# Kernel tuning notes

Measured on AMD Instinct MI355X. Metric: run time of the kernel, lower is better.

Reference implementation:

```python
import jax, jax.numpy as jnp
import numpy as np

N = 100000          # nodes
E = 1600000         # edges (avg degree 16)
F_NODE = 128        # num_node_features
F_EDGE = 32         # num_edge_features
HID = 128           # hidden_channels
OUT = 64            # out_channels


def setup_inputs() -> dict:
    key = jax.random.key(0)
    k = jax.random.split(key, 8)
    x = jax.random.normal(k[0], (N, F_NODE), dtype=jnp.float32)
    edge_index = jax.random.randint(k[1], (2, E), 0, N, dtype=jnp.int64)
    edge_attr = jax.random.normal(k[2], (E, F_EDGE), dtype=jnp.float32)
    # GCNConv parameters (lin weight + bias), glorot-ish scale
    w1 = jax.random.normal(k[3], (F_NODE + F_EDGE, HID), dtype=jnp.float32) * 0.05
    b1 = jnp.zeros((HID,), dtype=jnp.float32)
    w2 = jax.random.normal(k[4], (HID + F_EDGE, OUT), dtype=jnp.float32) * 0.05
    b2 = jnp.zeros((OUT,), dtype=jnp.float32)
    return {"x": x, "edge_index": edge_index, "edge_attr": edge_attr,
            "w1": w1, "b1": b1, "w2": w2, "b2": b2}


def _gcn_conv(h, src, dst, norm, w, b, num_nodes):
    # PyG GCNConv: linear transform, then normalized gather->scatter aggregation
    h = h @ w                                    # [N, out]
    msg = h[src] * norm[:, None]                 # gather at source nodes [E+N, out]
    out = jax.ops.segment_sum(msg, dst, num_segments=num_nodes)
    return out + b


def reference(x, edge_index, edge_attr, w1, b1, w2, b2):
    n = x.shape[0]
    row, col = edge_index[0], edge_index[1]

    # agg_edge_features.index_add_(0, row, edge_attr)
    agg = jax.ops.segment_sum(edge_attr, row, num_segments=n)  # [N, F_EDGE]

    # gcn_norm with self-loops (default GCNConv: add_self_loops=True, normalize=True)
    loop = jnp.arange(n, dtype=edge_index.dtype)
    src = jnp.concatenate([row, loop])
    dst = jnp.concatenate([col, loop])
    deg = jax.ops.segment_sum(jnp.ones(src.shape[0], dtype=x.dtype), dst,
                              num_segments=n)
    dinv = jnp.where(deg > 0, jax.lax.rsqrt(deg), jnp.zeros_like(deg))
    norm = dinv[src] * dinv[dst]                 # [E+N]

    h = jnp.concatenate([x, agg], axis=-1)       # [N, F_NODE+F_EDGE]
    h = _gcn_conv(h, src, dst, norm, w1, b1, n)
    h = jax.nn.relu(h)
    h = jnp.concatenate([h, agg], axis=-1)       # [N, HID+F_EDGE]
    out = _gcn_conv(h, src, dst, norm, w2, b2, n)
    return out
```

## Files before the change

### kernel.cpp

```cpp
#include <hip/hip_runtime.h>
#include <stdint.h>

#define F_NODE 128
#define F_EDGE 32
#define HID    128
#define OUTF   64

#define NBMAX  1024
#define CE     16384


__global__ void detect_kernel(const void* ei, int N, int* flag) {
    const long long* p64 = (const long long*)ei;
    int t = threadIdx.x;
    long long v = p64[t];
    int ok = (v >= 0 && v < (long long)N) ? 1 : 0;
    unsigned long long m = __ballot(ok);
    if (t == 0) *flag = (__popcll(m) >= 32) ? 1 : 0;
}

__global__ void decode_kernel(const void* ei, int E, int N, const int* flag,
                              int* __restrict__ row, int* __restrict__ col) {
    int i = blockIdx.x * blockDim.x + threadIdx.x;
    if (i >= E) return;
    int r, c;
    if (*flag) {
        const long long* p = (const long long*)ei;
        r = (int)p[i];
        c = (int)p[E + i];
    } else {
        const int* p = (const int*)ei;
        r = p[i];
        c = p[E + i];
    }
    r = min(max(r, 0), N - 1);
    c = min(max(c, 0), N - 1);
    row[i] = r;
    col[i] = c;
}

__global__ void zero_kernel(int* p, int n) {
    int i = blockIdx.x * blockDim.x + threadIdx.x;
    if (i < n) p[i] = 0;
}

__global__ void hist_kernel(const int* __restrict__ row, const int* __restrict__ col,
                            int E, int N, int* __restrict__ cnt) {
    int i = blockIdx.x * blockDim.x + threadIdx.x;
    if (i < E) {
        atomicAdd(&cnt[col[i]], 1);
        atomicAdd(&cnt[N + row[i]], 1);
    }
}

__global__ void scan1_kernel(const int* __restrict__ cnt, int M,
                             int* __restrict__ offs, int* __restrict__ bsum) {
    __shared__ int s[1024];
    int t = threadIdx.x;
    int i = blockIdx.x * 1024 + t;
    int v = (i < M) ? cnt[i] : 0;
    s[t] = v;
    __syncthreads();
    for (int d = 1; d < 1024; d <<= 1) {
        int x = (t >= d) ? s[t - d] : 0;
        __syncthreads();
        s[t] += x;
        __syncthreads();
    }
    if (i < M) offs[i + 1] = s[t];
    if (t == 1023) bsum[blockIdx.x] = s[1023];
}

__global__ void scan2_kernel(int* bsum, int nb) {
    __shared__ int s[1024];
    int t = threadIdx.x;
    int v = (t < nb) ? bsum[t] : 0;
    s[t] = v;
    __syncthreads();
    for (int d = 1; d < 1024; d <<= 1) {
        int x = (t >= d) ? s[t - d] : 0;
        __syncthreads();
        s[t] += x;
        __syncthreads();
    }
    if (t < nb) bsum[t] = s[t] - v;
}

__global__ void scan3_kernel(int* offs, int M, const int* __restrict__ bsum) {
    int i = blockIdx.x * blockDim.x + threadIdx.x;
    if (i == 0) offs[0] = 0;
    if (i < M) offs[i + 1] += bsum[i >> 10];
}

__global__ void dinv_kernel(const int* __restrict__ cnt, int N, float* __restrict__ dinv) {
    int i = blockIdx.x * blockDim.x + threadIdx.x;
    if (i < N) dinv[i] = rsqrtf((float)(cnt[i] + 1));
}

__global__ void coarse_cnt_kernel(const int* __restrict__ cnt, int N, int NB,
                                  int* __restrict__ ccnt) {
    __shared__ int s[128];
    int bi  = blockIdx.x;
    int srt = bi / NB;
    int b   = bi % NB;
    int idx = b * 128 + threadIdx.x;
    s[threadIdx.x] = (idx < N) ? cnt[srt * N + idx] : 0;
    __syncthreads();
    for (int d = 64; d > 0; d >>= 1) {
        if (threadIdx.x < d) s[threadIdx.x] += s[threadIdx.x + d];
        __syncthreads();
    }
    if (threadIdx.x == 0) ccnt[bi] = s[0];
}

__global__ void coarse_scan_kernel(const int* __restrict__ ccnt, int NB,
                                   int* __restrict__ cbase, int* __restrict__ ccur) {
    __shared__ int s[1024];
    int t = threadIdx.x;
    for (int seg = 0; seg < 2; ++seg) {
        int v = (t < NB) ? ccnt[seg * NB + t] : 0;
        s[t] = v;
        __syncthreads();
        for (int d = 1; d < 1024; d <<= 1) {
            int x = (t >= d) ? s[t - d] : 0;
            __syncthreads();
            s[t] += x;
            __syncthreads();
        }
        if (t < NB) {
            int ex = s[t] - v;
            cbase[seg * NB + t] = ex;
            ccur[seg * NB + t]  = ex;
        }
        __syncthreads();
    }
}

__global__ __launch_bounds__(256) void binscat_kernel(const int* __restrict__ row,
                                                      const int* __restrict__ col,
                                                      int E, int NB,
                                                      int* __restrict__ ccur,
                                                      int2* __restrict__ b1,
                                                      int2* __restrict__ b2) {
    __shared__ int histC[NBMAX], histR[NBMAX];
    __shared__ int baseC[NBMAX], baseR[NBMAX];
    __shared__ int curC[NBMAX],  curR[NBMAX];
    int t  = threadIdx.x;
    int e0 = blockIdx.x * CE;
    int e1 = min(e0 + CE, E);

    for (int b = t; b < NB; b += 256) { histC[b] = 0; histR[b] = 0; }
    __syncthreads();
    for (int i = e0 + t; i < e1; i += 256) {
        atomicAdd(&histC[col[i] >> 7], 1);
        atomicAdd(&histR[row[i] >> 7], 1);
    }
    __syncthreads();
    for (int b = t; b < NB; b += 256) {
        int hc = histC[b];
        if (hc) baseC[b] = atomicAdd(&ccur[b], hc);
        int hr = histR[b];
        if (hr) baseR[b] = atomicAdd(&ccur[NB + b], hr);
        curC[b] = 0;
        curR[b] = 0;
    }
    __syncthreads();
    for (int i = e0 + t; i < e1; i += 256) {
        int c = col[i], r = row[i];
        int bc = c >> 7, br = r >> 7;
        int rc = atomicAdd(&curC[bc], 1);
        b1[baseC[bc] + rc] = make_int2(c & 127, r);
        int rr = atomicAdd(&curR[br], 1);
        b2[baseR[br] + rr] = make_int2(r & 127, i);
    }
}

__global__ __launch_bounds__(256) void place_kernel(const int2* __restrict__ b1,
                                                    const int2* __restrict__ b2,
                                                    const int* __restrict__ cbase,
                                                    const int* __restrict__ ccnt,
                                                    const int* __restrict__ offs,
                                                    const float* __restrict__ dinv,
                                                    int N, int NB, int E,
                                                    int2* __restrict__ ent,
                                                    int* __restrict__ eid) {
    __shared__ int cur[128];
    int bi  = blockIdx.x;
    int srt = bi / NB;
    int bk  = bi % NB;
    int t   = threadIdx.x;
    if (t < 128) {
        int node = bk * 128 + t;
        if (node < N) cur[t] = (srt == 0) ? offs[node] : offs[N + node] - E;
    }
    __syncthreads();
    int base = cbase[bi], count = ccnt[bi];
    if (srt == 0) {
        for (int j = t; j < count; j += 256) {
            int2 e  = b1[base + j];
            int node = bk * 128 + e.x;
            int pos  = atomicAdd(&cur[e.x], 1);
            ent[pos] = make_int2(e.y, __float_as_int(dinv[e.y] * dinv[node]));
        }
    } else {
        for (int j = t; j < count; j += 256) {
            int2 e  = b2[base + j];
            int pos = atomicAdd(&cur[e.x], 1);
            eid[pos] = e.y;
        }
    }
}

__global__ __launch_bounds__(256) void aggr_kernel(const float* __restrict__ ea,
                                                   const int* __restrict__ offs,
                                                   const int* __restrict__ eid,
                                                   int N, int E,
                                                   float* __restrict__ agg) {
    int wid  = threadIdx.x >> 6;
    int lane = threadIdx.x & 63;
    int n = blockIdx.x * 4 + wid;
    if (n >= N) return;
    int f  = lane & 31;
    int hh = lane >> 5;
    int r0 = offs[N + n] - E;
    int r1 = offs[N + n + 1] - E;
    float s = 0.f;
    int e = r0 + hh;
    for (; e + 2 < r1; e += 4) {
        float x0 = ea[(size_t)eid[e] * F_EDGE + f];
        float x1 = ea[(size_t)eid[e + 2] * F_EDGE + f];
        s += x0 + x1;
    }
    if (e < r1) s += ea[(size_t)eid[e] * F_EDGE + f];
    s += __shfl(s, lane ^ 32);
    if (hh == 0) agg[(size_t)n * F_EDGE + f] = s;
}

template <int F, int BN, int TX>
__global__ __launch_bounds__(256) void gemm_kernel(const float* __restrict__ A,
                                                   const float* __restrict__ B,
                                                   const float* __restrict__ W,
                                                   float* __restrict__ outp, int N) {
    constexpr int TY  = 256 / TX;
    constexpr int NPT = BN / TY;
    constexpr int KC  = 32;
    constexpr int IST = KC + 4;
    constexpr int WST = F + 4;
    __shared__ float in_lds[BN][IST];
    __shared__ float w_lds[KC][WST];

    int t  = threadIdx.x;
    int tx = t % TX;
    int ty = t / TX;
    int n0 = blockIdx.x * BN;
    int j0 = tx * 8;

    float acc[NPT][8];
#pragma unroll
    for (int i = 0; i < NPT; ++i)
#pragma unroll
        for (int f = 0; f < 8; ++f) acc[i][f] = 0.f;

    for (int c = 0; c < 5; ++c) {
        const float* src = (c < 4) ? (A + c * KC) : B;
        int stride = (c < 4) ? F_NODE : F_EDGE;
        for (int l = t; l < BN * 8; l += 256) {
            int rr = l >> 3;
            int cc = (l & 7) * 4;
            int n = n0 + rr;
            if (n >= N) n = N - 1;
            float4 v = *(const float4*)(src + (size_t)n * stride + cc);
            *(float4*)&in_lds[rr][cc] = v;
        }
        for (int l = t; l < KC * F / 4; l += 256) {
            int rr = l / (F / 4);
            int cc = (l % (F / 4)) * 4;
            float4 v = *(const float4*)(W + (size_t)(c * KC + rr) * F + cc);
            *(float4*)&w_lds[rr][cc] = v;
        }
        __syncthreads();

#pragma unroll
        for (int kk = 0; kk < KC; kk += 4) {
            float4 a4[NPT];
#pragma unroll
            for (int i = 0; i < NPT; ++i)
                a4[i] = *(const float4*)&in_lds[ty * NPT + i][kk];
#pragma unroll
            for (int p = 0; p < 4; ++p) {
                float4 wa = *(const float4*)&w_lds[kk + p][j0];
                float4 wb = *(const float4*)&w_lds[kk + p][j0 + 4];
#pragma unroll
                for (int i = 0; i < NPT; ++i) {
                    float a = (p == 0) ? a4[i].x : (p == 1) ? a4[i].y
                              : (p == 2) ? a4[i].z : a4[i].w;
                    acc[i][0] = fmaf(a, wa.x, acc[i][0]);
                    acc[i][1] = fmaf(a, wa.y, acc[i][1]);
                    acc[i][2] = fmaf(a, wa.z, acc[i][2]);
                    acc[i][3] = fmaf(a, wa.w, acc[i][3]);
                    acc[i][4] = fmaf(a, wb.x, acc[i][4]);
                    acc[i][5] = fmaf(a, wb.y, acc[i][5]);
                    acc[i][6] = fmaf(a, wb.z, acc[i][6]);
                    acc[i][7] = fmaf(a, wb.w, acc[i][7]);
                }
            }
        }
        __syncthreads();
    }

#pragma unroll
    for (int i = 0; i < NPT; ++i) {
        int n = n0 + ty * NPT + i;
        if (n < N) {
            *(float4*)(outp + (size_t)n * F + j0) =
                make_float4(acc[i][0], acc[i][1], acc[i][2], acc[i][3]);
            *(float4*)(outp + (size_t)n * F + j0 + 4) =
                make_float4(acc[i][4], acc[i][5], acc[i][6], acc[i][7]);
        }
    }
}

template <int F, bool RELU>
__global__ __launch_bounds__(256) void conv_kernel(const float* __restrict__ h,
                                                   const int* __restrict__ offs,
                                                   const int2* __restrict__ ent,
                                                   const float* __restrict__ dinv,
                                                   const float* __restrict__ bias,
                                                   float* __restrict__ outp, int N) {
    int wid  = threadIdx.x >> 6;
    int lane = threadIdx.x & 63;
    int n = blockIdx.x * 4 + wid;
    if (n >= N) return;
    float dn = dinv[n];
    float sw = dn * dn;
    int e0 = offs[n], e1 = offs[n + 1];

    if constexpr (F == 128) {
        float2 hv = *((const float2*)(h + (size_t)n * F) + lane);
        float a0 = sw * hv.x, a1 = sw * hv.y;
        int e = e0;
        for (; e + 4 <= e1; e += 4) {
            int2 p0 = ent[e], p1 = ent[e + 1], p2 = ent[e + 2], p3 = ent[e + 3];
            float2 v0 = *((const float2*)(h + (size_t)p0.x * F) + lane);
            float2 v1 = *((const float2*)(h + (size_t)p1.x * F) + lane);
            float2 v2 = *((const float2*)(h + (size_t)p2.x * F) + lane);
            float2 v3 = *((const float2*)(h + (size_t)p3.x * F) + lane);
            float w0 = __int_as_float(p0.y), w1 = __int_as_float(p1.y);
            float w2 = __int_as_float(p2.y), w3 = __int_as_float(p3.y);
            a0 = fmaf(w0, v0.x, a0); a1 = fmaf(w0, v0.y, a1);
            a0 = fmaf(w1, v1.x, a0); a1 = fmaf(w1, v1.y, a1);
            a0 = fmaf(w2, v2.x, a0); a1 = fmaf(w2, v2.y, a1);
            a0 = fmaf(w3, v3.x, a0); a1 = fmaf(w3, v3.y, a1);
        }
        for (; e < e1; ++e) {
            int2 pr = ent[e];
            float w = __int_as_float(pr.y);
            float2 v = *((const float2*)(h + (size_t)pr.x * F) + lane);
            a0 = fmaf(w, v.x, a0);
            a1 = fmaf(w, v.y, a1);
        }
        float2 bv = *((const float2*)bias + lane);
        a0 += bv.x;
        a1 += bv.y;
        if (RELU) { a0 = fmaxf(a0, 0.f); a1 = fmaxf(a1, 0.f); }
        *((float2*)(outp + (size_t)n * F) + lane) = make_float2(a0, a1);
    } else {
        float a0 = sw * h[(size_t)n * F + lane];
        int e = e0;
        for (; e + 4 <= e1; e += 4) {
            int2 p0 = ent[e], p1 = ent[e + 1], p2 = ent[e + 2], p3 = ent[e + 3];
            float v0 = h[(size_t)p0.x * F + lane];
            float v1 = h[(size_t)p1.x * F + lane];
            float v2 = h[(size_t)p2.x * F + lane];
            float v3 = h[(size_t)p3.x * F + lane];
            a0 = fmaf(__int_as_float(p0.y), v0, a0);
            a0 = fmaf(__int_as_float(p1.y), v1, a0);
            a0 = fmaf(__int_as_float(p2.y), v2, a0);
            a0 = fmaf(__int_as_float(p3.y), v3, a0);
        }
        for (; e < e1; ++e) {
            int2 pr = ent[e];
            a0 = fmaf(__int_as_float(pr.y), h[(size_t)pr.x * F + lane], a0);
        }
        a0 += bias[lane];
        if (RELU) a0 = fmaxf(a0, 0.f);
        outp[(size_t)n * F + lane] = a0;
    }
}

extern "C" void kernel_launch(void* const* d_in, const int* in_sizes, int n_in,
                              void* d_out, int out_size, void* d_ws, size_t ws_size,
                              hipStream_t stream) {
    const float* x  = (const float*)d_in[0];
    const void*  ei = d_in[1];
    const float* ea = (const float*)d_in[2];
    const float* w1 = (const float*)d_in[3];
    const float* b1 = (const float*)d_in[4];
    const float* w2 = (const float*)d_in[5];
    const float* b2 = (const float*)d_in[6];
    float* out = (float*)d_out;

    int N = in_sizes[0] / F_NODE;
    int E = in_sizes[1] / 2;
    int NB = (N + 127) >> 7;

    char* ws = (char*)d_ws;
    size_t off = 0;
    auto alloc = [&](size_t bytes) -> void* {
        void* p = ws + off;
        off = (off + bytes + 255) & ~(size_t)255;
        return p;
    };

    int*   flag  = (int*)alloc(256);
    int*   row   = (int*)alloc((size_t)E * 4);
    int*   col   = (int*)alloc((size_t)E * 4);
    int*   cnt   = (int*)alloc((size_t)2 * N * 4);
    int*   offs  = (int*)alloc((size_t)(2 * N + 1) * 4);
    float* dinv  = (float*)alloc((size_t)N * 4);
    int*   bsum  = (int*)alloc(4096);
    int*   ccnt  = (int*)alloc((size_t)2 * NBMAX * 4);
    int*   cbase = (int*)alloc((size_t)2 * NBMAX * 4);
    int*   ccur  = (int*)alloc((size_t)2 * NBMAX * 4);
    int2*  ent   = (int2*)alloc((size_t)E * 8);
    int*   eid   = (int*)alloc((size_t)E * 4);
    float* agg   = (float*)alloc((size_t)N * F_EDGE * 4);
    float* h1    = (float*)alloc((size_t)N * HID * 4);
    float* hr    = (float*)alloc((size_t)N * HID * 4);
    float* h2    = (float*)alloc((size_t)N * OUTF * 4);

    int2* bkt1 = (int2*)h1;
    int2* bkt2 = (int2*)(h1 + (size_t)2 * E);

    int gE = (E + 255) / 256;
    int M  = 2 * N;
    int gM = (M + 255) / 256;
    int nb = (M + 1023) / 1024;

    detect_kernel<<<1, 64, 0, stream>>>(ei, N, flag);
    decode_kernel<<<gE, 256, 0, stream>>>(ei, E, N, flag, row, col);
    zero_kernel<<<gM, 256, 0, stream>>>(cnt, M);
    hist_kernel<<<gE, 256, 0, stream>>>(row, col, E, N, cnt);
    scan1_kernel<<<nb, 1024, 0, stream>>>(cnt, M, offs, bsum);
    scan2_kernel<<<1, 1024, 0, stream>>>(bsum, nb);
    scan3_kernel<<<gM, 256, 0, stream>>>(offs, M, bsum);
    dinv_kernel<<<(N + 255) / 256, 256, 0, stream>>>(cnt, N, dinv);
    coarse_cnt_kernel<<<2 * NB, 128, 0, stream>>>(cnt, N, NB, ccnt);
    coarse_scan_kernel<<<1, 1024, 0, stream>>>(ccnt, NB, cbase, ccur);
    binscat_kernel<<<(E + CE - 1) / CE, 256, 0, stream>>>(row, col, E, NB, ccur, bkt1, bkt2);
    place_kernel<<<2 * NB, 256, 0, stream>>>(bkt1, bkt2, cbase, ccnt, offs, dinv,
                                             N, NB, E, ent, eid);
    aggr_kernel<<<(N + 3) / 4, 256, 0, stream>>>(ea, offs, eid, N, E, agg);

    gemm_kernel<HID, 64, 16><<<(N + 63) / 64, 256, 0, stream>>>(x, agg, w1, h1, N);
    conv_kernel<HID, true><<<(N + 3) / 4, 256, 0, stream>>>(h1, offs, ent, dinv, b1, hr, N);
    gemm_kernel<OUTF, 128, 8><<<(N + 127) / 128, 256, 0, stream>>>(hr, agg, w2, h2, N);
    conv_kernel<OUTF, false><<<(N + 3) / 4, 256, 0, stream>>>(h2, offs, ent, dinv, b2, out, N);
}
```

Before: 911.1 us.

## Build CSR offsets per bucket and drop global histogram/scan passes

Fuses edge decoding with a coarse shared-memory bucket histogram, and removes the global per-node atomic histogram, the three-pass scan, the dinv kernel and the coarse count kernel. Per-node offsets and degree normalisation are now computed inside each bucket's build block via a local histogram and scan. Edge entries shrink from int2 (src, weight) to a plain int src, and the conv kernels recompute weights from dinv while unrolling the gather loop to 8. This trades fewer launches and global atomics, plus less CSR memory traffic, for an extra dinv gather per edge in the conv kernels.

```diff
diff --git a/kernel.cpp b/kernel.cpp
--- a/kernel.cpp
+++ b/kernel.cpp
@@ -19,98 +19,46 @@
     if (t == 0) *flag = (__popcll(m) >= 32) ? 1 : 0;
 }
 
-__global__ void decode_kernel(const void* ei, int E, int N, const int* flag,
-                              int* __restrict__ row, int* __restrict__ col) {
-    int i = blockIdx.x * blockDim.x + threadIdx.x;
-    if (i >= E) return;
-    int r, c;
-    if (*flag) {
-        const long long* p = (const long long*)ei;
-        r = (int)p[i];
-        c = (int)p[E + i];
-    } else {
-        const int* p = (const int*)ei;
-        r = p[i];
-        c = p[E + i];
-    }
-    r = min(max(r, 0), N - 1);
-    c = min(max(c, 0), N - 1);
-    row[i] = r;
-    col[i] = c;
-}
-
 __global__ void zero_kernel(int* p, int n) {
     int i = blockIdx.x * blockDim.x + threadIdx.x;
     if (i < n) p[i] = 0;
 }
 
-__global__ void hist_kernel(const int* __restrict__ row, const int* __restrict__ col,
-                            int E, int N, int* __restrict__ cnt) {
-    int i = blockIdx.x * blockDim.x + threadIdx.x;
-    if (i < E) {
-        atomicAdd(&cnt[col[i]], 1);
-        atomicAdd(&cnt[N + row[i]], 1);
-    }
-}
-
-__global__ void scan1_kernel(const int* __restrict__ cnt, int M,
-                             int* __restrict__ offs, int* __restrict__ bsum) {
-    __shared__ int s[1024];
+__global__ __launch_bounds__(256) void decode_hist_kernel(const void* ei, int E, int N,
+                                                          int NB, const int* flag,
+                                                          int* __restrict__ row,
+                                                          int* __restrict__ col,
+                                                          int* __restrict__ ccnt) {
+    __shared__ int hC[NBMAX], hR[NBMAX];
     int t = threadIdx.x;
-    int i = blockIdx.x * 1024 + t;
-    int v = (i < M) ? cnt[i] : 0;
-    s[t] = v;
-    __syncthreads();
-    for (int d = 1; d < 1024; d <<= 1) {
-        int x = (t >= d) ? s[t - d] : 0;
-        __syncthreads();
-        s[t] += x;
-        __syncthreads();
-    }
-    if (i < M) offs[i + 1] = s[t];
-    if (t == 1023) bsum[blockIdx.x] = s[1023];
-}
-
-__global__ void scan2_kernel(int* bsum, int nb) {
-    __shared__ int s[1024];
-    int t = threadIdx.x;
-    int v = (t < nb) ? bsum[t] : 0;
-    s[t] = v;
-    __syncthreads();
-    for (int d = 1; d < 1024; d <<= 1) {
-        int x = (t >= d) ? s[t - d] : 0;
-        __syncthreads();
-        s[t] += x;
-        __syncthreads();
-    }
-    if (t < nb) bsum[t] = s[t] - v;
-}
-
-__global__ void scan3_kernel(int* offs, int M, const int* __restrict__ bsum) {
-    int i = blockIdx.x * blockDim.x + threadIdx.x;
-    if (i == 0) offs[0] = 0;
-    if (i < M) offs[i + 1] += bsum[i >> 10];
-}
-
-__global__ void dinv_kernel(const int* __restrict__ cnt, int N, float* __restrict__ dinv) {
-    int i = blockIdx.x * blockDim.x + threadIdx.x;
-    if (i < N) dinv[i] = rsqrtf((float)(cnt[i] + 1));
-}
-
-__global__ void coarse_cnt_kernel(const int* __restrict__ cnt, int N, int NB,
-                                  int* __restrict__ ccnt) {
-    __shared__ int s[128];
-    int bi  = blockIdx.x;
-    int srt = bi / NB;
-    int b   = bi % NB;
-    int idx = b * 128 + threadIdx.x;
-    s[threadIdx.x] = (idx < N) ? cnt[srt * N + idx] : 0;
-    __syncthreads();
-    for (int d = 64; d > 0; d >>= 1) {
-        if (threadIdx.x < d) s[threadIdx.x] += s[threadIdx.x + d];
-        __syncthreads();
-    }
-    if (threadIdx.x == 0) ccnt[bi] = s[0];
+    for (int b = t; b < NB; b += 256) { hC[b] = 0; hR[b] = 0; }
+    __syncthreads();
+    int e0 = blockIdx.x * CE;
+    int e1 = min(e0 + CE, E);
+    bool wide = (*flag != 0);
+    for (int i = e0 + t; i < e1; i += 256) {
+        int r, c;
+        if (wide) {
+            const long long* p = (const long long*)ei;
+            r = (int)p[i];
+            c = (int)p[E + i];
+        } else {
+            const int* p = (const int*)ei;
+            r = p[i];
+            c = p[E + i];
+        }
+        r = min(max(r, 0), N - 1);
+        c = min(max(c, 0), N - 1);
+        row[i] = r;
+        col[i] = c;
+        atomicAdd(&hC[c >> 7], 1);
+        atomicAdd(&hR[r >> 7], 1);
+    }
+    __syncthreads();
+    for (int b = t; b < NB; b += 256) {
+        if (hC[b]) atomicAdd(&ccnt[b], hC[b]);
+        if (hR[b]) atomicAdd(&ccnt[NB + b], hR[b]);
+    }
 }
 
 __global__ void coarse_scan_kernel(const int* __restrict__ ccnt, int NB,
@@ -175,36 +123,65 @@
     }
 }
 
-__global__ __launch_bounds__(256) void place_kernel(const int2* __restrict__ b1,
+__global__ __launch_bounds__(256) void build_kernel(const int2* __restrict__ b1,
                                                     const int2* __restrict__ b2,
                                                     const int* __restrict__ cbase,
                                                     const int* __restrict__ ccnt,
-                                                    const int* __restrict__ offs,
-                                                    const float* __restrict__ dinv,
-                                                    int N, int NB, int E,
-                                                    int2* __restrict__ ent,
+                                                    int NB, int N, int E,
+                                                    int* __restrict__ doff,
+                                                    int* __restrict__ roff,
+                                                    float* __restrict__ dinv,
+                                                    int* __restrict__ ents,
                                                     int* __restrict__ eid) {
+    __shared__ int h[128];
+    __shared__ int sc[128];
     __shared__ int cur[128];
     int bi  = blockIdx.x;
     int srt = bi / NB;
     int bk  = bi % NB;
     int t   = threadIdx.x;
+    const int2* src = (srt == 0) ? b1 : b2;
+    int base  = cbase[bi];
+    int count = ccnt[bi];
+
+    if (t < 128) h[t] = 0;
+    __syncthreads();
+    for (int j = t; j < count; j += 256) atomicAdd(&h[src[base + j].x], 1);
+    __syncthreads();
+    if (t < 128) sc[t] = h[t];
+    __syncthreads();
+    for (int d = 1; d < 128; d <<= 1) {
+        int x = (t < 128 && t >= d) ? sc[t - d] : 0;
+        __syncthreads();
+        if (t < 128) sc[t] += x;
+        __syncthreads();
+    }
     if (t < 128) {
         int node = bk * 128 + t;
-        if (node < N) cur[t] = (srt == 0) ? offs[node] : offs[N + node] - E;
-    }
-    __syncthreads();
-    int base = cbase[bi], count = ccnt[bi];
+        if (node < N) {
+            int o = base + sc[t] - h[t];
+            cur[t] = o;
+            if (srt == 0) {
+                doff[node] = o;
+                dinv[node] = rsqrtf((float)(h[t] + 1));
+            } else {
+                roff[node] = o;
+            }
+        }
+    }
+    if (t == 0 && bk == 0) {
+        if (srt == 0) doff[N] = E; else roff[N] = E;
+    }
+    __syncthreads();
     if (srt == 0) {
         for (int j = t; j < count; j += 256) {
-            int2 e  = b1[base + j];
-            int node = bk * 128 + e.x;
-            int pos  = atomicAdd(&cur[e.x], 1);
-            ent[pos] = make_int2(e.y, __float_as_int(dinv[e.y] * dinv[node]));
+            int2 e = src[base + j];
+            int pos = atomicAdd(&cur[e.x], 1);
+            ents[pos] = e.y;
         }
     } else {
         for (int j = t; j < count; j += 256) {
-            int2 e  = b2[base + j];
+            int2 e = src[base + j];
             int pos = atomicAdd(&cur[e.x], 1);
             eid[pos] = e.y;
         }
@@ -212,9 +189,9 @@
 }
 
 __global__ __launch_bounds__(256) void aggr_kernel(const float* __restrict__ ea,
-                                                   const int* __restrict__ offs,
+                                                   const int* __restrict__ roff,
                                                    const int* __restrict__ eid,
-                                                   int N, int E,
+                                                   int N,
                                                    float* __restrict__ agg) {
     int wid  = threadIdx.x >> 6;
     int lane = threadIdx.x & 63;
@@ -222,8 +199,8 @@
     if (n >= N) return;
     int f  = lane & 31;
     int hh = lane >> 5;
-    int r0 = offs[N + n] - E;
-    int r1 = offs[N + n + 1] - E;
+    int r0 = roff[n];
+    int r1 = roff[n + 1];
     float s = 0.f;
     int e = r0 + hh;
     for (; e + 2 < r1; e += 4) {
@@ -322,8 +299,8 @@
 
 template <int F, bool RELU>
 __global__ __launch_bounds__(256) void conv_kernel(const float* __restrict__ h,
-                                                   const int* __restrict__ offs,
-                                                   const int2* __restrict__ ent,
+                                                   const int* __restrict__ doff,
+                                                   const int* __restrict__ ents,
                                                    const float* __restrict__ dinv,
                                                    const float* __restrict__ bias,
                                                    float* __restrict__ outp, int N) {
@@ -333,29 +310,53 @@
     if (n >= N) return;
     float dn = dinv[n];
     float sw = dn * dn;
-    int e0 = offs[n], e1 = offs[n + 1];
+    int e0 = doff[n], e1 = doff[n + 1];
 
     if constexpr (F == 128) {
         float2 hv = *((const float2*)(h + (size_t)n * F) + lane);
         float a0 = sw * hv.x, a1 = sw * hv.y;
         int e = e0;
-        for (; e + 4 <= e1; e += 4) {
-            int2 p0 = ent[e], p1 = ent[e + 1], p2 = ent[e + 2], p3 = ent[e + 3];
-            float2 v0 = *((const float2*)(h + (size_t)p0.x * F) + lane);
-            float2 v1 = *((const float2*)(h + (size_t)p1.x * F) + lane);
-            float2 v2 = *((const float2*)(h + (size_t)p2.x * F) + lane);
-            float2 v3 = *((const float2*)(h + (size_t)p3.x * F) + lane);
-            float w0 = __int_as_float(p0.y), w1 = __int_as_float(p1.y);
-            float w2 = __int_as_float(p2.y), w3 = __int_as_float(p3.y);
+        for (; e + 8 <= e1; e += 8) {
+            int s0 = ents[e],     s1 = ents[e + 1], s2 = ents[e + 2], s3 = ents[e + 3];
+            int s4 = ents[e + 4], s5 = ents[e + 5], s6 = ents[e + 6], s7 = ents[e + 7];
+            float2 v0 = *((const float2*)(h + (size_t)s0 * F) + lane);
+            float2 v1 = *((const float2*)(h + (size_t)s1 * F) + lane);
+            float2 v2 = *((const float2*)(h + (size_t)s2 * F) + lane);
+            float2 v3 = *((const float2*)(h + (size_t)s3 * F) + lane);
+            float2 v4 = *((const float2*)(h + (size_t)s4 * F) + lane);
+            float2 v5 = *((const float2*)(h + (size_t)s5 * F) + lane);
+            float2 v6 = *((const float2*)(h + (size_t)s6 * F) + lane);
+            float2 v7 = *((const float2*)(h + (size_t)s7 * F) + lane);
+            float w0 = dinv[s0] * dn, w1 = dinv[s1] * dn;
+            float w2 = dinv[s2] * dn, w3 = dinv[s3] * dn;
+            float w4 = dinv[s4] * dn, w5 = dinv[s5] * dn;
+            float w6 = dinv[s6] * dn, w7 = dinv[s7] * dn;
             a0 = fmaf(w0, v0.x, a0); a1 = fmaf(w0, v0.y, a1);
             a0 = fmaf(w1, v1.x, a0); a1 = fmaf(w1, v1.y, a1);
             a0 = fmaf(w2, v2.x, a0); a1 = fmaf(w2, v2.y, a1);
             a0 = fmaf(w3, v3.x, a0); a1 = fmaf(w3, v3.y, a1);
+            a0 = fmaf(w4, v4.x, a0); a1 = fmaf(w4, v4.y, a1);
+            a0 = fmaf(w5, v5.x, a0); a1 = fmaf(w5, v5.y, a1);
+            a0 = fmaf(w6, v6.x, a0); a1 = fmaf(w6, v6.y, a1);
+            a0 = fmaf(w7, v7.x, a0); a1 = fmaf(w7, v7.y, a1);
+        }
+        for (; e + 4 <= e1; e += 4) {
+            int s0 = ents[e], s1 = ents[e + 1], s2 = ents[e + 2], s3 = ents[e + 3];
+            float2 v0 = *((const float2*)(h + (size_t)s0 * F) + lane);
+            float2 v1 = *((const float2*)(h + (size_t)s1 * F) + lane);
+            float2 v2 = *((const float2*)(h + (size_t)s2 * F) + lane);
+            float2 v3 = *((const float2*)(h + (size_t)s3 * F) + lane);
+            float w0 = dinv[s0] * dn, w1 = dinv[s1] * dn;
+            float w2 = dinv[s2] * dn, w3 = dinv[s3] * dn;
+            a0 = fmaf(w0, v0.x, a0); a1 = fmaf(w0, v0.y, a1);
+            a0 = fmaf(w1, v1.x, a0); a1 = fmaf(w1, v1.y, a1);
+            a0 = fmaf(w2, v2.x, a0); a1 = fmaf(w2, v2.y, a1);
+            a0 = fmaf(w3, v3.x, a0); a1 = fmaf(w3, v3.y, a1);
         }
         for (; e < e1; ++e) {
-            int2 pr = ent[e];
-            float w = __int_as_float(pr.y);
-            float2 v = *((const float2*)(h + (size_t)pr.x * F) + lane);
+            int s = ents[e];
+            float w = dinv[s] * dn;
+            float2 v = *((const float2*)(h + (size_t)s * F) + lane);
             a0 = fmaf(w, v.x, a0);
             a1 = fmaf(w, v.y, a1);
         }
@@ -367,20 +368,40 @@
     } else {
         float a0 = sw * h[(size_t)n * F + lane];
         int e = e0;
+        for (; e + 8 <= e1; e += 8) {
+            int s0 = ents[e],     s1 = ents[e + 1], s2 = ents[e + 2], s3 = ents[e + 3];
+            int s4 = ents[e + 4], s5 = ents[e + 5], s6 = ents[e + 6], s7 = ents[e + 7];
+            float v0 = h[(size_t)s0 * F + lane];
+            float v1 = h[(size_t)s1 * F + lane];
+            float v2 = h[(size_t)s2 * F + lane];
+            float v3 = h[(size_t)s3 * F + lane];
+            float v4 = h[(size_t)s4 * F + lane];
+            float v5 = h[(size_t)s5 * F + lane];
+            float v6 = h[(size_t)s6 * F + lane];
+            float v7 = h[(size_t)s7 * F + lane];
+            a0 = fmaf(dinv[s0] * dn, v0, a0);
+            a0 = fmaf(dinv[s1] * dn, v1, a0);
+            a0 = fmaf(dinv[s2] * dn, v2, a0);
+            a0 = fmaf(dinv[s3] * dn, v3, a0);
+            a0 = fmaf(dinv[s4] * dn, v4, a0);
+            a0 = fmaf(dinv[s5] * dn, v5, a0);
+            a0 = fmaf(dinv[s6] * dn, v6, a0);
+            a0 = fmaf(dinv[s7] * dn, v7, a0);
+        }
         for (; e + 4 <= e1; e += 4) {
-            int2 p0 = ent[e], p1 = ent[e + 1], p2 = ent[e + 2], p3 = ent[e + 3];
-            float v0 = h[(size_t)p0.x * F + lane];
-            float v1 = h[(size_t)p1.x * F + lane];
-            float v2 = h[(size_t)p2.x * F + lane];
-            float v3 = h[(size_t)p3.x * F + lane];
-            a0 = fmaf(__int_as_float(p0.y), v0, a0);
-            a0 = fmaf(__int_as_float(p1.y), v1, a0);
-            a0 = fmaf(__int_as_float(p2.y), v2, a0);
-            a0 = fmaf(__int_as_float(p3.y), v3, a0);
+            int s0 = ents[e], s1 = ents[e + 1], s2 = ents[e + 2], s3 = ents[e + 3];
+            float v0 = h[(size_t)s0 * F + lane];
+            float v1 = h[(size_t)s1 * F + lane];
+            float v2 = h[(size_t)s2 * F + lane];
+            float v3 = h[(size_t)s3 * F + lane];
+            a0 = fmaf(dinv[s0] * dn, v0, a0);
+            a0 = fmaf(dinv[s1] * dn, v1, a0);
+            a0 = fmaf(dinv[s2] * dn, v2, a0);
+            a0 = fmaf(dinv[s3] * dn, v3, a0);
         }
         for (; e < e1; ++e) {
-            int2 pr = ent[e];
-            a0 = fmaf(__int_as_float(pr.y), h[(size_t)pr.x * F + lane], a0);
+            int s = ents[e];
+            a0 = fmaf(dinv[s] * dn, h[(size_t)s * F + lane], a0);
         }
         a0 += bias[lane];
         if (RELU) a0 = fmaxf(a0, 0.f);
@@ -415,14 +436,13 @@
     int*   flag  = (int*)alloc(256);
     int*   row   = (int*)alloc((size_t)E * 4);
     int*   col   = (int*)alloc((size_t)E * 4);
-    int*   cnt   = (int*)alloc((size_t)2 * N * 4);
-    int*   offs  = (int*)alloc((size_t)(2 * N + 1) * 4);
-    float* dinv  = (float*)alloc((size_t)N * 4);
-    int*   bsum  = (int*)alloc(4096);
     int*   ccnt  = (int*)alloc((size_t)2 * NBMAX * 4);
     int*   cbase = (int*)alloc((size_t)2 * NBMAX * 4);
     int*   ccur  = (int*)alloc((size_t)2 * NBMAX * 4);
-    int2*  ent   = (int2*)alloc((size_t)E * 8);
+    int*   doff  = (int*)alloc((size_t)(N + 1) * 4);
+    int*   roff  = (int*)alloc((size_t)(N + 1) * 4);
+    float* dinv  = (float*)alloc((size_t)N * 4);
+    int*   ents  = (int*)alloc((size_t)E * 4);
     int*   eid   = (int*)alloc((size_t)E * 4);
     float* agg   = (float*)alloc((size_t)N * F_EDGE * 4);
     float* h1    = (float*)alloc((size_t)N * HID * 4);
@@ -432,28 +452,19 @@
     int2* bkt1 = (int2*)h1;
     int2* bkt2 = (int2*)(h1 + (size_t)2 * E);
 
-    int gE = (E + 255) / 256;
-    int M  = 2 * N;
-    int gM = (M + 255) / 256;
-    int nb = (M + 1023) / 1024;
+    int nChunk = (E + CE - 1) / CE;
 
     detect_kernel<<<1, 64, 0, stream>>>(ei, N, flag);
-    decode_kernel<<<gE, 256, 0, stream>>>(ei, E, N, flag, row, col);
-    zero_kernel<<<gM, 256, 0, stream>>>(cnt, M);
-    hist_kernel<<<gE, 256, 0, stream>>>(row, col, E, N, cnt);
-    scan1_kernel<<<nb, 1024, 0, stream>>>(cnt, M, offs, bsum);
-    scan2_kernel<<<1, 1024, 0, stream>>>(bsum, nb);
-    scan3_kernel<<<gM, 256, 0, stream>>>(offs, M, bsum);
-    dinv_kernel<<<(N + 255) / 256, 256, 0, stream>>>(cnt, N, dinv);
-    coarse_cnt_kernel<<<2 * NB, 128, 0, stream>>>(cnt, N, NB, ccnt);
+    zero_kernel<<<(2 * NB + 255) / 256, 256, 0, stream>>>(ccnt, 2 * NB);
+    decode_hist_kernel<<<nChunk, 256, 0, stream>>>(ei, E, N, NB, flag, row, col, ccnt);
     coarse_scan_kernel<<<1, 1024, 0, stream>>>(ccnt, NB, cbase, ccur);
-    binscat_kernel<<<(E + CE - 1) / CE, 256, 0, stream>>>(row, col, E, NB, ccur, bkt1, bkt2);
-    place_kernel<<<2 * NB, 256, 0, stream>>>(bkt1, bkt2, cbase, ccnt, offs, dinv,
-                                             N, NB, E, ent, eid);
-    aggr_kernel<<<(N + 3) / 4, 256, 0, stream>>>(ea, offs, eid, N, E, agg);
+    binscat_kernel<<<nChunk, 256, 0, stream>>>(row, col, E, NB, ccur, bkt1, bkt2);
+    build_kernel<<<2 * NB, 256, 0, stream>>>(bkt1, bkt2, cbase, ccnt, NB, N, E,
+                                             doff, roff, dinv, ents, eid);
+    aggr_kernel<<<(N + 3) / 4, 256, 0, stream>>>(ea, roff, eid, N, agg);
 
     gemm_kernel<HID, 64, 16><<<(N + 63) / 64, 256, 0, stream>>>(x, agg, w1, h1, N);
-    conv_kernel<HID, true><<<(N + 3) / 4, 256, 0, stream>>>(h1, offs, ent, dinv, b1, hr, N);
+    conv_kernel<HID, true><<<(N + 3) / 4, 256, 0, stream>>>(h1, doff, ents, dinv, b1, hr, N);
     gemm_kernel<OUTF, 128, 8><<<(N + 127) / 128, 256, 0, stream>>>(hr, agg, w2, h2, N);
-    conv_kernel<OUTF, false><<<(N + 3) / 4, 256, 0, stream>>>(h2, offs, ent, dinv, b2, out, N);
-}
+    conv_kernel<OUTF, false><<<(N + 3) / 4, 256, 0, stream>>>(h2, doff, ents, dinv, b2, out, N);
+}
```

New measurement: 791.5 us. 13.1% less time.
